# Kernel optimization log

Hardware: AMD Instinct MI355X
Metric: run time of the kernel (lower is better)

The kernel has to match this reference:

```python
import jax, jax.numpy as jnp
import numpy as np

B, T, C, H = 8, 1024, 1024, 16
NEG = -1000000000.0
EPS = 1e-12


def setup_inputs() -> dict:
    key = jax.random.key(0)
    ks = jax.random.split(key, 12)
    s = 0.02  # keep pre-softmax logits in a sane range
    return {
        "x": jax.random.normal(ks[0], (B, T, C), jnp.float32),
        "mask": jax.random.randint(ks[1], (B, T), 0, 2, jnp.int32),
        "Wq": jax.random.normal(ks[2], (C, C), jnp.float32) * s,
        "bq": jax.random.normal(ks[3], (C,), jnp.float32) * s,
        "Wk": jax.random.normal(ks[4], (C, C), jnp.float32) * s,
        "bk": jax.random.normal(ks[5], (C,), jnp.float32) * s,
        "Wv": jax.random.normal(ks[6], (C, C), jnp.float32) * s,
        "bv": jax.random.normal(ks[7], (C,), jnp.float32) * s,
        "Wp": jax.random.normal(ks[8], (C, C), jnp.float32) * s,
        "bp": jax.random.normal(ks[9], (C,), jnp.float32) * s,
        "ln_w": jnp.ones((C,), jnp.float32),
        "ln_b": jnp.zeros((C,), jnp.float32),
    }


def reference(x, mask, Wq, bq, Wk, bk, Wv, bv, Wp, bp, ln_w, ln_b):
    Bx, Tx, Cx = x.shape
    hd = Cx // H
    # torch nn.Linear: y = x @ W.T + b
    def lin(inp, W, b):
        return inp @ W.T + b

    def split_heads(t):  # [B,T,C] -> [B,H,T,hd]
        return t.reshape(Bx, Tx, H, hd).transpose(0, 2, 1, 3)

    q = split_heads(lin(x, Wq, bq))
    k = split_heads(lin(x, Wk, bk))
    v = split_heads(lin(x, Wv, bv))

    att = jnp.einsum("bhqd,bhkd->bhqk", q, k) * (1.0 / jnp.sqrt(jnp.float32(hd)))
    # mask [B,T] masks key positions; broadcast to [B,1,1,T]
    att = jnp.where(mask[:, None, None, :] == 0, NEG, att)
    # stable softmax (manual max-subtract, matching original)
    att = jax.nn.softmax(att, axis=-1)
    # dropout prob 0.0 -> identity (eval-mode faithful)
    y = jnp.einsum("bhqk,bhkd->bhqd", att, v)
    y = y.transpose(0, 2, 1, 3).reshape(Bx, Tx, Cx)
    y = lin(y, Wp, bp)
    # residual + LayerNorm(eps=1e-12)
    z = y + x
    mu = jnp.mean(z, axis=-1, keepdims=True)
    var = jnp.mean(jnp.square(z - mu), axis=-1, keepdims=True)
    out = (z - mu) * jax.lax.rsqrt(var + EPS) * ln_w + ln_b
    return out
```

## Files before the change

kernel.cpp:

```cpp
#include <hip/hip_runtime.h>
#include <stdint.h>

#define B_ 8
#define T_ 1024
#define C_ 1024
#define H_ 16
#define HD 64
#define M_TOT (B_ * T_)

using f32x4 = __attribute__((ext_vector_type(4))) float;
using s16x8 = __attribute__((ext_vector_type(8))) short;
using i32x4 = __attribute__((ext_vector_type(4))) int;

__device__ __forceinline__ unsigned short f2bf(float f) {
  unsigned int u = __builtin_bit_cast(unsigned int, f);
  unsigned int r = (u + 0x7fffu + ((u >> 16) & 1u)) >> 16;
  return (unsigned short)r;
}

__device__ __forceinline__ void gload_lds16(const void* g, void* l) {
  __builtin_amdgcn_global_load_lds(
      (const __attribute__((address_space(1))) unsigned int*)g,
      (__attribute__((address_space(3))) unsigned int*)l, 16, 0, 0);
}

__global__ __launch_bounds__(256) void k_convert(
    const float* __restrict__ x, const float* __restrict__ wq,
    const float* __restrict__ wk, const float* __restrict__ wv,
    const float* __restrict__ wp, const float* __restrict__ bq,
    const float* __restrict__ bk, const float* __restrict__ bv,
    const int* __restrict__ maskp, unsigned short* __restrict__ xb,
    unsigned short* __restrict__ wqkv, unsigned short* __restrict__ wpb,
    float* __restrict__ bias_cat, unsigned int* __restrict__ mpair) {
  const long n_x = (long)M_TOT * C_;
  const long W_ELT = (long)C_ * C_;
  const long total4 = (n_x + 4 * W_ELT) >> 2;
  for (long i4 = (long)blockIdx.x * blockDim.x + threadIdx.x; i4 < total4;
       i4 += (long)gridDim.x * blockDim.x) {
    long i = i4 << 2;
    const float* src;
    unsigned short* dst;
    if (i < n_x) {
      src = x + i;
      dst = xb + i;
    } else {
      long off = i - n_x;
      int which = (int)(off >> 20);
      long wo = off & (W_ELT - 1);
      if (which < 3) {
        src = (which == 0 ? wq : which == 1 ? wk : wv) + wo;
        dst = wqkv + which * W_ELT + wo;
      } else {
        src = wp + wo;
        dst = wpb + wo;
      }
    }
    float4 v = *(const float4*)src;
    ushort4 u;
    u.x = f2bf(v.x); u.y = f2bf(v.y); u.z = f2bf(v.z); u.w = f2bf(v.w);
    *(ushort4*)dst = u;
  }
  int t = blockIdx.x * blockDim.x + threadIdx.x;
  if (t < 3 * C_) {
    float v = t < C_ ? bq[t] : (t < 2 * C_ ? bk[t - C_] : bv[t - 2 * C_]);
    bias_cat[t] = v;
  }
  if (t < B_ * T_ / 2) {
    const int* mr = maskp + t * 2;
    mpair[t] = (mr[0] ? 0xFFFFu : 0u) | (mr[1] ? 0xFFFF0000u : 0u);
  }
}

template <int EPI>
__global__ __launch_bounds__(256, 2) void k_gemm(
    const unsigned short* __restrict__ A, const unsigned short* __restrict__ Bm,
    const float* __restrict__ bias, unsigned short* __restrict__ q_ws,
    unsigned short* __restrict__ k_ws, unsigned short* __restrict__ vt_ws,
    const float* __restrict__ xres, float* __restrict__ zout) {
  __shared__ unsigned short Al[2][128 * 64];
  __shared__ unsigned short Bl[2][128 * 64];
  const int tid = threadIdx.x, lane = tid & 63, w = tid >> 6;
  const int lc = lane & 15, lr = lane >> 4;
  const int wm = w >> 1, wn = w & 1;
  const int GX = (EPI == 0) ? 24 : 8;
  const int NWG = GX * 64;
  int flat = blockIdx.y * GX + blockIdx.x;
  int swz = (flat & 7) * (NWG / 8) + (flat >> 3);
  const int m0 = (swz / GX) * 128, n0 = (swz % GX) * 128;
  const char* Ab = (const char*)A;
  const char* Bb = (const char*)Bm;

  f32x4 acc[4][4] = {};

  auto stage = [&](int buf, int kt) {
#pragma unroll
    for (int i = 0; i < 4; ++i) {
      int g = i * 256 + tid;
      int row = g >> 3, gr = g & 7;
      gload_lds16(Ab + (long)(m0 + row) * 2048 + kt * 128 + ((gr ^ (row & 7)) << 4),
                  (char*)Al[buf] + (i * 256 + w * 64) * 16);
    }
#pragma unroll
    for (int i = 0; i < 4; ++i) {
      int g = i * 256 + tid;
      int row = g >> 3, gr = g & 7;
      gload_lds16(Bb + (long)(n0 + row) * 2048 + kt * 128 + ((gr ^ (row & 7)) << 4),
                  (char*)Bl[buf] + (i * 256 + w * 64) * 16);
    }
  };

  stage(0, 0);
  stage(1, 1);
  asm volatile("s_waitcnt vmcnt(8)" ::: "memory");
  __builtin_amdgcn_sched_barrier(0);
  __builtin_amdgcn_s_barrier();
  __builtin_amdgcn_sched_barrier(0);

#pragma unroll
  for (int kt = 0; kt < 16; ++kt) {
    const int cur = kt & 1;
    const char* Ac = (const char*)Al[cur];
    const char* Bc = (const char*)Bl[cur];
    s16x8 af0[4], bf0[4];
#pragma unroll
    for (int mf = 0; mf < 4; ++mf) {
      int ar = wm * 64 + mf * 16 + lc;
      af0[mf] = *(const s16x8*)(Ac + ar * 128 + ((lr ^ (ar & 7)) << 4));
    }
#pragma unroll
    for (int nf = 0; nf < 4; ++nf) {
      int br = wn * 64 + nf * 16 + lc;
      bf0[nf] = *(const s16x8*)(Bc + br * 128 + ((lr ^ (br & 7)) << 4));
    }
#pragma unroll
    for (int mf = 0; mf < 4; ++mf)
#pragma unroll
      for (int nf = 0; nf < 4; ++nf)
        acc[mf][nf] = __builtin_amdgcn_mfma_f32_16x16x32_bf16(af0[mf], bf0[nf],
                                                              acc[mf][nf], 0, 0, 0);
    s16x8 af1[4], bf1[4];
#pragma unroll
    for (int mf = 0; mf < 4; ++mf) {
      int ar = wm * 64 + mf * 16 + lc;
      af1[mf] = *(const s16x8*)(Ac + ar * 128 + (((4 + lr) ^ (ar & 7)) << 4));
    }
#pragma unroll
    for (int nf = 0; nf < 4; ++nf) {
      int br = wn * 64 + nf * 16 + lc;
      bf1[nf] = *(const s16x8*)(Bc + br * 128 + (((4 + lr) ^ (br & 7)) << 4));
    }
    asm volatile("s_waitcnt lgkmcnt(0)" ::: "memory");
    __builtin_amdgcn_sched_barrier(0);
    __builtin_amdgcn_s_barrier();
    __builtin_amdgcn_sched_barrier(0);
    if (kt + 2 < 16) stage(cur, kt + 2);
    __builtin_amdgcn_s_setprio(1);
#pragma unroll
    for (int mf = 0; mf < 4; ++mf)
#pragma unroll
      for (int nf = 0; nf < 4; ++nf)
        acc[mf][nf] = __builtin_amdgcn_mfma_f32_16x16x32_bf16(af1[mf], bf1[nf],
                                                              acc[mf][nf], 0, 0, 0);
    __builtin_amdgcn_s_setprio(0);
    if (kt + 2 < 16)
      asm volatile("s_waitcnt vmcnt(8)" ::: "memory");
    else
      asm volatile("s_waitcnt vmcnt(0)" ::: "memory");
    __builtin_amdgcn_sched_barrier(0);
    __builtin_amdgcn_s_barrier();
    __builtin_amdgcn_sched_barrier(0);
  }

  if (EPI == 0) {
#pragma unroll
    for (int mf = 0; mf < 4; ++mf)
#pragma unroll
      for (int nf = 0; nf < 4; ++nf) {
        int gn = n0 + wn * 64 + nf * 16 + lc;
        int which = gn >> 10, nn = gn & 1023;
        int hh = nn >> 6, dd = nn & 63;
        float bia = bias[gn];
        if (which == 2) {
          int gm = m0 + wm * 64 + mf * 16 + lr * 4;
          int bb = gm >> 10, tt = gm & 1023;
          ushort4 pk;
          pk.x = f2bf(acc[mf][nf][0] + bia);
          pk.y = f2bf(acc[mf][nf][1] + bia);
          pk.z = f2bf(acc[mf][nf][2] + bia);
          pk.w = f2bf(acc[mf][nf][3] + bia);
          *(ushort4*)&vt_ws[((long)(bb * H_ + hh) * HD + dd) * T_ + tt] = pk;
        } else {
          unsigned short* dst = (which == 0) ? q_ws : k_ws;
          float scl = (which == 0) ? 0.18033688011112042f : 1.0f;
#pragma unroll
          for (int i = 0; i < 4; ++i) {
            int gm = m0 + wm * 64 + mf * 16 + lr * 4 + i;
            int bb = gm >> 10, tt = gm & 1023;
            dst[((long)(bb * H_ + hh) * T_ + tt) * HD + dd] =
                f2bf((acc[mf][nf][i] + bia) * scl);
          }
        }
      }
  } else {
#pragma unroll
    for (int mf = 0; mf < 4; ++mf)
#pragma unroll
      for (int nf = 0; nf < 4; ++nf) {
        int gn = n0 + wn * 64 + nf * 16 + lc;
        float bia = bias[gn];
#pragma unroll
        for (int i = 0; i < 4; ++i) {
          int gm = m0 + wm * 64 + mf * 16 + lr * 4 + i;
          long idx = (long)gm * C_ + gn;
          zout[idx] = acc[mf][nf][i] + bia + xres[idx];
        }
      }
  }
}

__global__ __launch_bounds__(512, 4) void k_attn(
    const unsigned short* __restrict__ Qp, const unsigned short* __restrict__ Kp,
    const unsigned short* __restrict__ Vtp, const unsigned int* __restrict__ mpairp,
    unsigned short* __restrict__ Yp) {
  __shared__ unsigned short Kl[2][64 * 64];
  __shared__ unsigned short Vl[2][64 * 64];
  const int tid = threadIdx.x, lane = tid & 63, w = tid >> 6;
  const int bid = blockIdx.x;
  const int xcd = bid & 7, slot = bid >> 3;
  const int bh = xcd * 16 + (slot >> 3);
  const int qt = slot & 7;
  const int b = bh >> 4, h = bh & 15;
  const int lc = lane & 15, lr = lane >> 4;
  const int q0 = qt * 128 + w * 16;

  const unsigned short* qbase = Qp + ((long)bh * T_ + q0) * HD;
  s16x8 aq0 = *(const s16x8*)(qbase + lc * HD + lr * 8);
  s16x8 aq1 = *(const s16x8*)(qbase + lc * HD + 32 + lr * 8);

  s16x8 ones;
#pragma unroll
  for (int j = 0; j < 8; ++j) ones[j] = (short)0x3F80;

  f32x4 o[4] = {};
  f32x4 o_l = {};

  const char* kb_g = (const char*)(Kp + (long)bh * T_ * HD);
  const char* vb_g = (const char*)(Vtp + (long)bh * HD * T_);
  const unsigned int* mrow2 = mpairp + b * (T_ / 2);

  auto stage = [&](int buf, int kt) {
    int f = tid * 16;
    int row = f >> 7;
    int swz = (f & 127) ^ ((row & 7) << 4);
    gload_lds16(kb_g + (long)kt * 8192 + (f & ~127) + swz,
                (char*)Kl[buf] + w * 1024);
    gload_lds16(vb_g + (long)row * (T_ * 2) + kt * 128 + swz,
                (char*)Vl[buf] + w * 1024);
  };

  stage(0, 0);
  __syncthreads();

  const int s01 = lc + ((lane & 16) << 1);
  const int s23 = s01 + 16;
  const bool hi = (lane >= 32);

  int cur = 0;
  for (int kt = 0; kt < T_ / 64; ++kt) {
    if (kt + 1 < T_ / 64) stage(cur ^ 1, kt + 1);

    f32x4 s[4];
    const char* kl = (const char*)Kl[cur];
#pragma unroll
    for (int kf = 0; kf < 4; ++kf) {
      int key = kf * 16 + lc;
      s16x8 kb0 = *(const s16x8*)(kl + ((key * 128 + lr * 16) ^ ((key & 7) << 4)));
      s16x8 kb1 = *(const s16x8*)(kl + ((key * 128 + 64 + lr * 16) ^ ((key & 7) << 4)));
      f32x4 z = {};
      z = __builtin_amdgcn_mfma_f32_16x16x32_bf16(kb0, aq0, z, 0, 0, 0);
      z = __builtin_amdgcn_mfma_f32_16x16x32_bf16(kb1, aq1, z, 0, 0, 0);
      s[kf] = z;
    }

    unsigned int mw[4][2];
#pragma unroll
    for (int kf = 0; kf < 4; ++kf) {
      mw[kf][0] = mrow2[kt * 32 + kf * 8 + lr * 2];
      mw[kf][1] = mrow2[kt * 32 + kf * 8 + lr * 2 + 1];
    }

    unsigned int pk[4][2];
#pragma unroll
    for (int kf = 0; kf < 4; ++kf) {
      float p0 = __builtin_amdgcn_exp2f(s[kf][0]);
      float p1 = __builtin_amdgcn_exp2f(s[kf][1]);
      float p2 = __builtin_amdgcn_exp2f(s[kf][2]);
      float p3 = __builtin_amdgcn_exp2f(s[kf][3]);
      unsigned int u0 = __builtin_bit_cast(unsigned int, p0);
      unsigned int u1 = __builtin_bit_cast(unsigned int, p1);
      unsigned int u2 = __builtin_bit_cast(unsigned int, p2);
      unsigned int u3 = __builtin_bit_cast(unsigned int, p3);
      pk[kf][0] = ((u1 & 0xFFFF0000u) | (u0 >> 16)) & mw[kf][0];
      pk[kf][1] = ((u3 & 0xFFFF0000u) | (u2 >> 16)) & mw[kf][1];
    }

    s16x8 ap[2];
#pragma unroll
    for (int kc = 0; kc < 2; ++kc) {
      unsigned int A0 = pk[kc * 2][0], A1 = pk[kc * 2][1];
      unsigned int B0 = pk[kc * 2 + 1][0], B1 = pk[kc * 2 + 1][1];
      unsigned int w0a = __shfl((int)A0, s01, 64), w0b = __shfl((int)B0, s01, 64);
      unsigned int w1a = __shfl((int)A1, s01, 64), w1b = __shfl((int)B1, s01, 64);
      unsigned int w2a = __shfl((int)A0, s23, 64), w2b = __shfl((int)B0, s23, 64);
      unsigned int w3a = __shfl((int)A1, s23, 64), w3b = __shfl((int)B1, s23, 64);
      i32x4 wv;
      wv[0] = (int)(hi ? w0b : w0a);
      wv[1] = (int)(hi ? w1b : w1a);
      wv[2] = (int)(hi ? w2b : w2a);
      wv[3] = (int)(hi ? w3b : w3a);
      ap[kc] = __builtin_bit_cast(s16x8, wv);
    }

#pragma unroll
    for (int kc = 0; kc < 2; ++kc) {
      int koff = kc * 64 + lr * 16;
      o_l = __builtin_amdgcn_mfma_f32_16x16x32_bf16(ones, ap[kc], o_l, 0, 0, 0);
#pragma unroll
      for (int nf = 0; nf < 4; ++nf) {
        int drow = nf * 16 + lc;
        s16x8 vb = *(const s16x8*)((const char*)Vl[cur] +
                                   ((drow * 128 + koff) ^ ((drow & 7) << 4)));
        o[nf] = __builtin_amdgcn_mfma_f32_16x16x32_bf16(vb, ap[kc], o[nf], 0, 0, 0);
      }
    }
    __syncthreads();
    cur ^= 1;
  }

  float rl = 1.0f / o_l[0];
  unsigned short* yrow = Yp + ((long)(b * T_ + q0 + lc)) * C_ + h * 64;
#pragma unroll
  for (int nf = 0; nf < 4; ++nf) {
    ushort4 pw;
    pw.x = f2bf(o[nf][0] * rl);
    pw.y = f2bf(o[nf][1] * rl);
    pw.z = f2bf(o[nf][2] * rl);
    pw.w = f2bf(o[nf][3] * rl);
    *(ushort4*)(yrow + nf * 16 + lr * 4) = pw;
  }
}

__global__ __launch_bounds__(256) void k_ln(const float* __restrict__ z,
                                            const float* __restrict__ lw,
                                            const float* __restrict__ lb,
                                            float* __restrict__ out) {
  const int row = blockIdx.x;
  float4 v = ((const float4*)(z + (long)row * C_))[threadIdx.x];
  float s = v.x + v.y + v.z + v.w;
  float s2 = v.x * v.x + v.y * v.y + v.z * v.z + v.w * v.w;
#pragma unroll
  for (int d = 1; d < 64; d <<= 1) {
    s += __shfl_xor(s, d, 64);
    s2 += __shfl_xor(s2, d, 64);
  }
  __shared__ float rs[4], rq[4];
  int wv_ = threadIdx.x >> 6;
  if ((threadIdx.x & 63) == 0) { rs[wv_] = s; rq[wv_] = s2; }
  __syncthreads();
  s = rs[0] + rs[1] + rs[2] + rs[3];
  s2 = rq[0] + rq[1] + rq[2] + rq[3];
  float mu = s * (1.0f / C_);
  float var = s2 * (1.0f / C_) - mu * mu;
  float inv = rsqrtf(var + 1e-12f);
  float4 wv4 = ((const float4*)lw)[threadIdx.x];
  float4 bv4 = ((const float4*)lb)[threadIdx.x];
  float4 ov;
  ov.x = (v.x - mu) * inv * wv4.x + bv4.x;
  ov.y = (v.y - mu) * inv * wv4.y + bv4.y;
  ov.z = (v.z - mu) * inv * wv4.z + bv4.z;
  ov.w = (v.w - mu) * inv * wv4.w + bv4.w;
  ((float4*)(out + (long)row * C_))[threadIdx.x] = ov;
}

extern "C" void kernel_launch(void* const* d_in, const int* in_sizes, int n_in,
                              void* d_out, int out_size, void* d_ws,
                              size_t ws_size, hipStream_t stream) {
  const float* x = (const float*)d_in[0];
  const int* mask = (const int*)d_in[1];
  const float* Wq = (const float*)d_in[2];
  const float* bq = (const float*)d_in[3];
  const float* Wk = (const float*)d_in[4];
  const float* bk = (const float*)d_in[5];
  const float* Wv = (const float*)d_in[6];
  const float* bv = (const float*)d_in[7];
  const float* Wp = (const float*)d_in[8];
  const float* bp = (const float*)d_in[9];
  const float* lnw = (const float*)d_in[10];
  const float* lnb = (const float*)d_in[11];
  float* out = (float*)d_out;

  char* ws = (char*)d_ws;
  const size_t MB = 1024 * 1024;
  unsigned short* xb = (unsigned short*)(ws);
  unsigned short* q_ws = (unsigned short*)(ws + 16 * MB);
  unsigned short* k_ws = (unsigned short*)(ws + 32 * MB);
  unsigned short* vt_ws = (unsigned short*)(ws + 48 * MB);
  unsigned short* y_ws = (unsigned short*)(ws + 64 * MB);
  unsigned short* wqkv = (unsigned short*)(ws + 80 * MB);
  unsigned short* wpb = (unsigned short*)(ws + 86 * MB);
  float* bias_cat = (float*)(ws + 88 * MB);
  unsigned int* mpair = (unsigned int*)(ws + 88 * MB + 16384);
  float* z = (float*)(ws);

  k_convert<<<dim3(2048), dim3(256), 0, stream>>>(x, Wq, Wk, Wv, Wp, bq, bk, bv,
                                                  mask, xb, wqkv, wpb, bias_cat,
                                                  mpair);
  k_gemm<0><<<dim3(24, 64), dim3(256), 0, stream>>>(
      xb, wqkv, bias_cat, q_ws, k_ws, vt_ws, nullptr, nullptr);
  k_attn<<<dim3(1024), dim3(512), 0, stream>>>(q_ws, k_ws, vt_ws, mpair, y_ws);
  k_gemm<1><<<dim3(8, 64), dim3(256), 0, stream>>>(
      y_ws, wpb, bp, nullptr, nullptr, nullptr, x, z);
  k_ln<<<dim3(8192), dim3(256), 0, stream>>>(z, lnw, lnb, out);
}
```

Measured before the change: 176.2 us.

## Process two query tiles per wave in attention to reuse K/V fragments

```diff
diff --git a/kernel.cpp b/kernel.cpp
--- a/kernel.cpp
+++ b/kernel.cpp
@@ -227,22 +227,24 @@
   const int tid = threadIdx.x, lane = tid & 63, w = tid >> 6;
   const int bid = blockIdx.x;
   const int xcd = bid & 7, slot = bid >> 3;
-  const int bh = xcd * 16 + (slot >> 3);
-  const int qt = slot & 7;
+  const int bh = xcd * 16 + (slot >> 2);
+  const int qt = slot & 3;
   const int b = bh >> 4, h = bh & 15;
   const int lc = lane & 15, lr = lane >> 4;
-  const int q0 = qt * 128 + w * 16;
+  const int q0 = qt * 256 + w * 32;
 
   const unsigned short* qbase = Qp + ((long)bh * T_ + q0) * HD;
-  s16x8 aq0 = *(const s16x8*)(qbase + lc * HD + lr * 8);
-  s16x8 aq1 = *(const s16x8*)(qbase + lc * HD + 32 + lr * 8);
+  s16x8 aqA0 = *(const s16x8*)(qbase + lc * HD + lr * 8);
+  s16x8 aqA1 = *(const s16x8*)(qbase + lc * HD + 32 + lr * 8);
+  s16x8 aqB0 = *(const s16x8*)(qbase + (16 + lc) * HD + lr * 8);
+  s16x8 aqB1 = *(const s16x8*)(qbase + (16 + lc) * HD + 32 + lr * 8);
 
   s16x8 ones;
 #pragma unroll
   for (int j = 0; j < 8; ++j) ones[j] = (short)0x3F80;
 
-  f32x4 o[4] = {};
-  f32x4 o_l = {};
+  f32x4 oA[4] = {}, oB[4] = {};
+  f32x4 olA = {}, olB = {};
 
   const char* kb_g = (const char*)(Kp + (long)bh * T_ * HD);
   const char* vb_g = (const char*)(Vtp + (long)bh * HD * T_);
@@ -269,17 +271,20 @@
   for (int kt = 0; kt < T_ / 64; ++kt) {
     if (kt + 1 < T_ / 64) stage(cur ^ 1, kt + 1);
 
-    f32x4 s[4];
+    f32x4 sA[4], sB[4];
     const char* kl = (const char*)Kl[cur];
 #pragma unroll
     for (int kf = 0; kf < 4; ++kf) {
       int key = kf * 16 + lc;
       s16x8 kb0 = *(const s16x8*)(kl + ((key * 128 + lr * 16) ^ ((key & 7) << 4)));
       s16x8 kb1 = *(const s16x8*)(kl + ((key * 128 + 64 + lr * 16) ^ ((key & 7) << 4)));
-      f32x4 z = {};
-      z = __builtin_amdgcn_mfma_f32_16x16x32_bf16(kb0, aq0, z, 0, 0, 0);
-      z = __builtin_amdgcn_mfma_f32_16x16x32_bf16(kb1, aq1, z, 0, 0, 0);
-      s[kf] = z;
+      f32x4 zA = {}, zB = {};
+      zA = __builtin_amdgcn_mfma_f32_16x16x32_bf16(kb0, aqA0, zA, 0, 0, 0);
+      zB = __builtin_amdgcn_mfma_f32_16x16x32_bf16(kb0, aqB0, zB, 0, 0, 0);
+      zA = __builtin_amdgcn_mfma_f32_16x16x32_bf16(kb1, aqA1, zA, 0, 0, 0);
+      zB = __builtin_amdgcn_mfma_f32_16x16x32_bf16(kb1, aqB1, zB, 0, 0, 0);
+      sA[kf] = zA;
+      sB[kf] = zB;
     }
 
     unsigned int mw[4][2];
@@ -289,64 +294,89 @@
       mw[kf][1] = mrow2[kt * 32 + kf * 8 + lr * 2 + 1];
     }
 
-    unsigned int pk[4][2];
+    unsigned int pkA[4][2], pkB[4][2];
 #pragma unroll
     for (int kf = 0; kf < 4; ++kf) {
-      float p0 = __builtin_amdgcn_exp2f(s[kf][0]);
-      float p1 = __builtin_amdgcn_exp2f(s[kf][1]);
-      float p2 = __builtin_amdgcn_exp2f(s[kf][2]);
-      float p3 = __builtin_amdgcn_exp2f(s[kf][3]);
-      unsigned int u0 = __builtin_bit_cast(unsigned int, p0);
-      unsigned int u1 = __builtin_bit_cast(unsigned int, p1);
-      unsigned int u2 = __builtin_bit_cast(unsigned int, p2);
-      unsigned int u3 = __builtin_bit_cast(unsigned int, p3);
-      pk[kf][0] = ((u1 & 0xFFFF0000u) | (u0 >> 16)) & mw[kf][0];
-      pk[kf][1] = ((u3 & 0xFFFF0000u) | (u2 >> 16)) & mw[kf][1];
-    }
-
-    s16x8 ap[2];
+#pragma unroll
+      for (int g = 0; g < 2; ++g) {
+        const f32x4& sv = g ? sB[kf] : sA[kf];
+        unsigned int u0 = __builtin_bit_cast(unsigned int, __builtin_amdgcn_exp2f(sv[0]));
+        unsigned int u1 = __builtin_bit_cast(unsigned int, __builtin_amdgcn_exp2f(sv[1]));
+        unsigned int u2 = __builtin_bit_cast(unsigned int, __builtin_amdgcn_exp2f(sv[2]));
+        unsigned int u3 = __builtin_bit_cast(unsigned int, __builtin_amdgcn_exp2f(sv[3]));
+        unsigned int w0 = ((u1 & 0xFFFF0000u) | (u0 >> 16)) & mw[kf][0];
+        unsigned int w1 = ((u3 & 0xFFFF0000u) | (u2 >> 16)) & mw[kf][1];
+        if (g) { pkB[kf][0] = w0; pkB[kf][1] = w1; }
+        else   { pkA[kf][0] = w0; pkA[kf][1] = w1; }
+      }
+    }
+
 #pragma unroll
     for (int kc = 0; kc < 2; ++kc) {
-      unsigned int A0 = pk[kc * 2][0], A1 = pk[kc * 2][1];
-      unsigned int B0 = pk[kc * 2 + 1][0], B1 = pk[kc * 2 + 1][1];
-      unsigned int w0a = __shfl((int)A0, s01, 64), w0b = __shfl((int)B0, s01, 64);
-      unsigned int w1a = __shfl((int)A1, s01, 64), w1b = __shfl((int)B1, s01, 64);
-      unsigned int w2a = __shfl((int)A0, s23, 64), w2b = __shfl((int)B0, s23, 64);
-      unsigned int w3a = __shfl((int)A1, s23, 64), w3b = __shfl((int)B1, s23, 64);
-      i32x4 wv;
-      wv[0] = (int)(hi ? w0b : w0a);
-      wv[1] = (int)(hi ? w1b : w1a);
-      wv[2] = (int)(hi ? w2b : w2a);
-      wv[3] = (int)(hi ? w3b : w3a);
-      ap[kc] = __builtin_bit_cast(s16x8, wv);
-    }
-
-#pragma unroll
-    for (int kc = 0; kc < 2; ++kc) {
+      s16x8 apA, apB;
+      {
+        unsigned int A0 = pkA[kc * 2][0], A1 = pkA[kc * 2][1];
+        unsigned int B0 = pkA[kc * 2 + 1][0], B1 = pkA[kc * 2 + 1][1];
+        unsigned int w0a = __shfl((int)A0, s01, 64), w0b = __shfl((int)B0, s01, 64);
+        unsigned int w1a = __shfl((int)A1, s01, 64), w1b = __shfl((int)B1, s01, 64);
+        unsigned int w2a = __shfl((int)A0, s23, 64), w2b = __shfl((int)B0, s23, 64);
+        unsigned int w3a = __shfl((int)A1, s23, 64), w3b = __shfl((int)B1, s23, 64);
+        i32x4 wv;
+        wv[0] = (int)(hi ? w0b : w0a);
+        wv[1] = (int)(hi ? w1b : w1a);
+        wv[2] = (int)(hi ? w2b : w2a);
+        wv[3] = (int)(hi ? w3b : w3a);
+        apA = __builtin_bit_cast(s16x8, wv);
+      }
+      {
+        unsigned int A0 = pkB[kc * 2][0], A1 = pkB[kc * 2][1];
+        unsigned int B0 = pkB[kc * 2 + 1][0], B1 = pkB[kc * 2 + 1][1];
+        unsigned int w0a = __shfl((int)A0, s01, 64), w0b = __shfl((int)B0, s01, 64);
+        unsigned int w1a = __shfl((int)A1, s01, 64), w1b = __shfl((int)B1, s01, 64);
+        unsigned int w2a = __shfl((int)A0, s23, 64), w2b = __shfl((int)B0, s23, 64);
+        unsigned int w3a = __shfl((int)A1, s23, 64), w3b = __shfl((int)B1, s23, 64);
+        i32x4 wv;
+        wv[0] = (int)(hi ? w0b : w0a);
+        wv[1] = (int)(hi ? w1b : w1a);
+        wv[2] = (int)(hi ? w2b : w2a);
+        wv[3] = (int)(hi ? w3b : w3a);
+        apB = __builtin_bit_cast(s16x8, wv);
+      }
       int koff = kc * 64 + lr * 16;
-      o_l = __builtin_amdgcn_mfma_f32_16x16x32_bf16(ones, ap[kc], o_l, 0, 0, 0);
+      __builtin_amdgcn_s_setprio(1);
+      olA = __builtin_amdgcn_mfma_f32_16x16x32_bf16(ones, apA, olA, 0, 0, 0);
+      olB = __builtin_amdgcn_mfma_f32_16x16x32_bf16(ones, apB, olB, 0, 0, 0);
 #pragma unroll
       for (int nf = 0; nf < 4; ++nf) {
         int drow = nf * 16 + lc;
         s16x8 vb = *(const s16x8*)((const char*)Vl[cur] +
                                    ((drow * 128 + koff) ^ ((drow & 7) << 4)));
-        o[nf] = __builtin_amdgcn_mfma_f32_16x16x32_bf16(vb, ap[kc], o[nf], 0, 0, 0);
-      }
+        oA[nf] = __builtin_amdgcn_mfma_f32_16x16x32_bf16(vb, apA, oA[nf], 0, 0, 0);
+        oB[nf] = __builtin_amdgcn_mfma_f32_16x16x32_bf16(vb, apB, oB[nf], 0, 0, 0);
+      }
+      __builtin_amdgcn_s_setprio(0);
     }
     __syncthreads();
     cur ^= 1;
   }
 
-  float rl = 1.0f / o_l[0];
-  unsigned short* yrow = Yp + ((long)(b * T_ + q0 + lc)) * C_ + h * 64;
+  float rlA = 1.0f / olA[0];
+  float rlB = 1.0f / olB[0];
+  unsigned short* yrowA = Yp + ((long)(b * T_ + q0 + lc)) * C_ + h * 64;
+  unsigned short* yrowB = Yp + ((long)(b * T_ + q0 + 16 + lc)) * C_ + h * 64;
 #pragma unroll
   for (int nf = 0; nf < 4; ++nf) {
-    ushort4 pw;
-    pw.x = f2bf(o[nf][0] * rl);
-    pw.y = f2bf(o[nf][1] * rl);
-    pw.z = f2bf(o[nf][2] * rl);
-    pw.w = f2bf(o[nf][3] * rl);
-    *(ushort4*)(yrow + nf * 16 + lr * 4) = pw;
+    ushort4 pwA, pwB;
+    pwA.x = f2bf(oA[nf][0] * rlA);
+    pwA.y = f2bf(oA[nf][1] * rlA);
+    pwA.z = f2bf(oA[nf][2] * rlA);
+    pwA.w = f2bf(oA[nf][3] * rlA);
+    pwB.x = f2bf(oB[nf][0] * rlB);
+    pwB.y = f2bf(oB[nf][1] * rlB);
+    pwB.z = f2bf(oB[nf][2] * rlB);
+    pwB.w = f2bf(oB[nf][3] * rlB);
+    *(ushort4*)(yrowA + nf * 16 + lr * 4) = pwA;
+    *(ushort4*)(yrowB + nf * 16 + lr * 4) = pwB;
   }
 }
 
@@ -417,7 +447,7 @@
                                                   mpair);
   k_gemm<0><<<dim3(24, 64), dim3(256), 0, stream>>>(
       xb, wqkv, bias_cat, q_ws, k_ws, vt_ws, nullptr, nullptr);
-  k_attn<<<dim3(1024), dim3(512), 0, stream>>>(q_ws, k_ws, vt_ws, mpair, y_ws);
+  k_attn<<<dim3(512), dim3(512), 0, stream>>>(q_ws, k_ws, vt_ws, mpair, y_ws);
   k_gemm<1><<<dim3(8, 64), dim3(256), 0, stream>>>(
       y_ws, wpb, bp, nullptr, nullptr, nullptr, x, z);
   k_ln<<<dim3(8192), dim3(256), 0, stream>>>(z, lnw, lnb, out);
```

After: 164.7 us. 6.5% less time.
